# Kernel tuning notes

Hardware: AMD Instinct MI355X
Metric: run time of the kernel (lower is better)

Reference implementation:

```python
import jax, jax.numpy as jnp
import numpy as np

S, B, HQ, HK, D = 2048, 2, 32, 8, 128


def setup_inputs() -> dict:
    key = jax.random.key(0)
    kq, kk, kv = jax.random.split(key, 3)
    return {
        "query": jax.random.normal(kq, (S, B, HQ, D), dtype=jnp.float32),
        "key": jax.random.normal(kk, (S, B, HK, D), dtype=jnp.float32),
        "value": jax.random.normal(kv, (S, B, HK, D), dtype=jnp.float32),
    }


def reference(query, key, value):
    # s b h d -> b s h d (module's rearrange)
    q = jnp.transpose(query, (1, 0, 2, 3))  # [B,S,HQ,D]
    k = jnp.transpose(key, (1, 0, 2, 3))    # [B,S,HK,D]
    v = jnp.transpose(value, (1, 0, 2, 3))
    n_rep = q.shape[2] // k.shape[2]
    # repeat_kv: GQA expand along head dim (repeat_interleave semantics)
    k = jnp.repeat(k, n_rep, axis=2)  # [B,S,HQ,D]
    v = jnp.repeat(v, n_rep, axis=2)
    scale = q.shape[-1] ** -0.5
    # [B,H,Sq,Sk] scores; causal mask
    scores = jnp.einsum("bqhd,bkhd->bhqk", q, k) * scale
    s = scores.shape[-1]
    causal = jnp.tril(jnp.ones((s, s), dtype=bool))
    scores = jnp.where(causal[None, None], scores, jnp.finfo(scores.dtype).min)
    probs = jax.nn.softmax(scores, axis=-1)
    out = jnp.einsum("bhqk,bkhd->bqhd", probs, v)  # [B,S,H,D]
    # back to Megatron output layout [s, b, h*d]
    out = jnp.transpose(out, (1, 0, 2, 3))
    return out.reshape(out.shape[0], out.shape[1], -1)
```

## Files before the change

kernel.cpp:

```cpp
#include <hip/hip_runtime.h>

#define SLEN 2048
#define NB 2
#define NHQ 32
#define NHK 8
#define DH 128
#define QBLK 128
#define KVBLK 64
#define NT (SLEN / KVBLK)
#define NQT (SLEN / QBLK)
#define TILE_B (KVBLK * DH * 2)

typedef float  f32x4  __attribute__((ext_vector_type(4)));
typedef short  bf16x8 __attribute__((ext_vector_type(8)));

__device__ __forceinline__ unsigned short f2bf(float f) {
  union { float f; unsigned int u; } v; v.f = f;
  return (unsigned short)((v.u + 0x7fffu + ((v.u >> 16) & 1u)) >> 16);
}

__device__ __forceinline__ unsigned int cvtpk(float a, float b) {
  unsigned int r;
  asm("v_cvt_pk_bf16_f32 %0, %1, %2" : "=v"(r) : "v"(a), "v"(b));
  return r;
}

#define GLOAD16(g, l)                                                                   \
  __builtin_amdgcn_global_load_lds(                                                    \
      (const __attribute__((address_space(1))) unsigned int*)(g),                      \
      (__attribute__((address_space(3))) unsigned int*)(l), 16, 0, 0)

__global__ __launch_bounds__(256)
void prep_kv(const float* __restrict__ K, const float* __restrict__ V,
             unsigned short* __restrict__ W) {
  const int tile = blockIdx.x;
  const int bh   = blockIdx.y;
  const int tid  = threadIdx.x;
  const size_t krs = (size_t)NB * NHK * DH;
  const float* kb = K + (size_t)bh * DH + (size_t)tile * KVBLK * krs;
  const float* vb = V + (size_t)bh * DH + (size_t)tile * KVBLK * krs;
  unsigned short* kd = W + ((size_t)bh * NT + tile) * (KVBLK * DH);
  unsigned short* vd = W + (size_t)NB * NHK * NT * (KVBLK * DH)
                         + ((size_t)bh * NT + tile) * (KVBLK * DH);
#pragma unroll
  for (int i = 0; i < 4; ++i) {
    const int cid  = tid + 256 * i;
    const int row  = cid >> 4;
    const int cpos = (cid & 15) << 4;
    const int cb   = cpos ^ ((row & 7) << 4);
    const float* s = kb + (size_t)row * krs + (cb >> 1);
    float4 f0 = *(const float4*)s;
    float4 f1 = *(const float4*)(s + 4);
    bf16x8 a;
    a[0]=(short)f2bf(f0.x); a[1]=(short)f2bf(f0.y); a[2]=(short)f2bf(f0.z); a[3]=(short)f2bf(f0.w);
    a[4]=(short)f2bf(f1.x); a[5]=(short)f2bf(f1.y); a[6]=(short)f2bf(f1.z); a[7]=(short)f2bf(f1.w);
    *(bf16x8*)((char*)kd + row * 256 + cpos) = a;
  }
#pragma unroll
  for (int i = 0; i < 4; ++i) {
    const int cid  = tid + 256 * i;
    const int d    = cid >> 3;
    const int cpos = (cid & 7) << 4;
    const int kb2  = cpos ^ ((d & 7) << 4);
    const int p0   = kb2 >> 1;
    bf16x8 a;
#pragma unroll
    for (int j = 0; j < 8; ++j) {
      const int p  = p0 + j;
      const int kv = (p & 32) | ((p & 4) << 2) | ((p & 24) >> 1) | (p & 3);
      a[j] = (short)f2bf(vb[(size_t)kv * krs + d]);
    }
    *(bf16x8*)((char*)vd + d * 128 + cpos) = a;
  }
}

__global__ __launch_bounds__(256, 3)
void fattn_fwd(const float* __restrict__ Q, const unsigned short* __restrict__ KW,
               const unsigned short* __restrict__ VW, float* __restrict__ O) {
  const int tid  = threadIdx.x;
  const int w    = tid >> 6;
  const int lane = tid & 63;
  const int l15  = lane & 15;
  const int g    = lane >> 4;

  const int wg  = (int)blockIdx.x;
  const int xcd = wg & 7;
  const int c0  = wg >> 3;
  const int bh  = 8 * xcd + (c0 & 7);
  const int qt  = (NQT - 1) - (c0 >> 3);
  const int b   = bh >> 5;
  const int h   = bh & (NHQ - 1);
  const int kh  = h >> 2;

  __shared__ alignas(16) unsigned short Kbuf[2][KVBLK * DH];
  __shared__ alignas(16) unsigned short Vbuf[DH * KVBLK];

  const char* kws = (const char*)(KW + ((size_t)(b * NHK + kh) * NT) * (KVBLK * DH));
  const char* vws = (const char*)(VW + ((size_t)(b * NHK + kh) * NT) * (KVBLK * DH));

  const float sc = 0.08838834764831845f * 1.4426950408889634f;

  const int qs0 = qt * QBLK + 32 * w;
  const int nt  = 2 * qt + 2;

  bf16x8 qa[2][4];
#pragma unroll
  for (int u = 0; u < 2; ++u) {
    const float* qp = Q + ((size_t)((qs0 + 16 * u + l15) * NB + b) * NHQ + h) * DH;
#pragma unroll
    for (int s = 0; s < 4; ++s) {
      const float* p = qp + 32 * s + 8 * g;
      float4 f0 = *(const float4*)(p);
      float4 f1 = *(const float4*)(p + 4);
      bf16x8 a;
      a[0]=(short)f2bf(f0.x*sc); a[1]=(short)f2bf(f0.y*sc);
      a[2]=(short)f2bf(f0.z*sc); a[3]=(short)f2bf(f0.w*sc);
      a[4]=(short)f2bf(f1.x*sc); a[5]=(short)f2bf(f1.y*sc);
      a[6]=(short)f2bf(f1.z*sc); a[7]=(short)f2bf(f1.w*sc);
      qa[u][s] = a;
    }
  }

  bf16x8 ones;
#pragma unroll
  for (int i = 0; i < 8; ++i) ones[i] = (short)0x3F80;

  f32x4 o[2][8];
#pragma unroll
  for (int u = 0; u < 2; ++u)
#pragma unroll
    for (int dt = 0; dt < 8; ++dt) o[u][dt] = (f32x4){0.f, 0.f, 0.f, 0.f};
  f32x4 lacc[2] = {(f32x4){0.f,0.f,0.f,0.f}, (f32x4){0.f,0.f,0.f,0.f}};

#pragma unroll
  for (int i = 0; i < 4; ++i) {
    const int off = i * 4096 + w * 1024;
    GLOAD16(kws + off + (lane << 4), (char*)Kbuf[0] + off);
  }

  int cur = 0;
  for (int it = 0; it < nt; ++it) {
    {
      const char* vs = vws + (size_t)it * TILE_B;
#pragma unroll
      for (int i = 0; i < 4; ++i) {
        const int off = i * 4096 + w * 1024;
        GLOAD16(vs + off + (lane << 4), (char*)Vbuf + off);
      }
    }
    if (it + 1 < nt) {
      const char* ks = kws + (size_t)(it + 1) * TILE_B;
#pragma unroll
      for (int i = 0; i < 4; ++i) {
        const int off = i * 4096 + w * 1024;
        GLOAD16(ks + off + (lane << 4), (char*)Kbuf[cur ^ 1] + off);
      }
      asm volatile("s_waitcnt vmcnt(8)" ::: "memory");
    } else {
      asm volatile("s_waitcnt vmcnt(4)" ::: "memory");
    }
    __builtin_amdgcn_s_barrier();
    asm volatile("" ::: "memory");

    const unsigned short* Kc = Kbuf[cur];
    const int kv0 = it * KVBLK;
    const bool live = (kv0 <= qs0 + 31);

    f32x4 acc[2][4];
    bf16x8 pav[2][2];
    if (live) {
#pragma unroll
      for (int u = 0; u < 2; ++u)
#pragma unroll
        for (int c = 0; c < 4; ++c) acc[u][c] = (f32x4){0.f, 0.f, 0.f, 0.f};
      __builtin_amdgcn_s_setprio(1);
#pragma unroll
      for (int s = 0; s < 4; ++s) {
        const int cb = 64 * s + 16 * g;
#pragma unroll
        for (int c = 0; c < 4; ++c) {
          const int row = 16 * c + l15;
          bf16x8 kfr = *(const bf16x8*)((const char*)Kc + row * 256 + (cb ^ ((row & 7) << 4)));
          acc[0][c] = __builtin_amdgcn_mfma_f32_16x16x32_bf16(kfr, qa[0][s], acc[0][c], 0, 0, 0);
          acc[1][c] = __builtin_amdgcn_mfma_f32_16x16x32_bf16(kfr, qa[1][s], acc[1][c], 0, 0, 0);
        }
      }
      __builtin_amdgcn_s_setprio(0);

#pragma unroll
      for (int u = 0; u < 2; ++u) {
        const int qs   = qs0 + 16 * u;
        const int qrow = qs + l15;
        const bool domask = (kv0 + KVBLK - 1 > qs);
        float p[4][4];
#pragma unroll
        for (int c = 0; c < 4; ++c)
#pragma unroll
          for (int r = 0; r < 4; ++r) {
            float v = acc[u][c][r];
            if (domask) {
              const int kv = kv0 + 16 * c + 4 * g + r;
              v = (kv > qrow) ? -1e30f : v;
            }
            p[c][r] = exp2f(v);
          }

#pragma unroll
        for (int ks = 0; ks < 2; ++ks) {
          union { unsigned int u32[4]; bf16x8 v; } pu;
          pu.u32[0] = cvtpk(p[2 * ks][0], p[2 * ks][1]);
          pu.u32[1] = cvtpk(p[2 * ks][2], p[2 * ks][3]);
          pu.u32[2] = cvtpk(p[2 * ks + 1][0], p[2 * ks + 1][1]);
          pu.u32[3] = cvtpk(p[2 * ks + 1][2], p[2 * ks + 1][3]);
          pav[u][ks] = pu.v;
        }
      }

      lacc[0] = __builtin_amdgcn_mfma_f32_16x16x32_bf16(ones, pav[0][0], lacc[0], 0, 0, 0);
      lacc[0] = __builtin_amdgcn_mfma_f32_16x16x32_bf16(ones, pav[0][1], lacc[0], 0, 0, 0);
      lacc[1] = __builtin_amdgcn_mfma_f32_16x16x32_bf16(ones, pav[1][0], lacc[1], 0, 0, 0);
      lacc[1] = __builtin_amdgcn_mfma_f32_16x16x32_bf16(ones, pav[1][1], lacc[1], 0, 0, 0);
    }

    if (it + 1 < nt) {
      asm volatile("s_waitcnt vmcnt(4)" ::: "memory");
    } else {
      asm volatile("s_waitcnt vmcnt(0)" ::: "memory");
    }
    __builtin_amdgcn_s_barrier();
    asm volatile("" ::: "memory");

    if (live) {
      __builtin_amdgcn_s_setprio(1);
#pragma unroll
      for (int ks = 0; ks < 2; ++ks) {
#pragma unroll
        for (int dt = 0; dt < 8; ++dt) {
          const int d = 16 * dt + l15;
          bf16x8 vfr = *(const bf16x8*)((const char*)Vbuf + d * 128 +
                                        ((64 * ks + 16 * g) ^ ((d & 7) << 4)));
          o[0][dt] = __builtin_amdgcn_mfma_f32_16x16x32_bf16(vfr, pav[0][ks], o[0][dt], 0, 0, 0);
          o[1][dt] = __builtin_amdgcn_mfma_f32_16x16x32_bf16(vfr, pav[1][ks], o[1][dt], 0, 0, 0);
        }
      }
      __builtin_amdgcn_s_setprio(0);
    }

    asm volatile("" ::: "memory");
    __builtin_amdgcn_s_barrier();
    cur ^= 1;
  }

#pragma unroll
  for (int u = 0; u < 2; ++u) {
    const float rl = 1.0f / lacc[u][0];
    const int qrow = qs0 + 16 * u + l15;
    float* ob = O + ((size_t)b * NHQ + h) * DH + (size_t)qrow * (NB * NHQ * DH);
#pragma unroll
    for (int dt = 0; dt < 8; ++dt) {
      float4 st;
      st.x = o[u][dt][0] * rl; st.y = o[u][dt][1] * rl;
      st.z = o[u][dt][2] * rl; st.w = o[u][dt][3] * rl;
      *(float4*)(ob + 16 * dt + 4 * g) = st;
    }
  }
}

extern "C" void kernel_launch(void* const* d_in, const int* in_sizes, int n_in,
                              void* d_out, int out_size, void* d_ws, size_t ws_size,
                              hipStream_t stream) {
  const float* Q = (const float*)d_in[0];
  const float* K = (const float*)d_in[1];
  const float* V = (const float*)d_in[2];
  float* Out = (float*)d_out;
  unsigned short* W = (unsigned short*)d_ws;

  dim3 pgrid(NT, NB * NHK);
  prep_kv<<<pgrid, 256, 0, stream>>>(K, V, W);

  const unsigned short* KW = W;
  const unsigned short* VW = W + (size_t)NB * NHK * NT * (KVBLK * DH);
  fattn_fwd<<<dim3(NQT * NB * NHQ), 256, 0, stream>>>(Q, KW, VW, Out);
}
```

Measured before the change: 120.4 us.

## Split V tile into LDS-staged half and register-loaded half, double-buffer V

```diff
diff --git a/kernel.cpp b/kernel.cpp
--- a/kernel.cpp
+++ b/kernel.cpp
@@ -9,7 +9,8 @@
 #define KVBLK 64
 #define NT (SLEN / KVBLK)
 #define NQT (SLEN / QBLK)
-#define TILE_B (KVBLK * DH * 2)
+#define KTILE_B (KVBLK * DH * 2)
+#define VTILE_B (KVBLK * DH)
 
 typedef float  f32x4  __attribute__((ext_vector_type(4)));
 typedef short  bf16x8 __attribute__((ext_vector_type(8)));
@@ -32,16 +33,17 @@
 
 __global__ __launch_bounds__(256)
 void prep_kv(const float* __restrict__ K, const float* __restrict__ V,
-             unsigned short* __restrict__ W) {
+             unsigned short* __restrict__ KW, unsigned short* __restrict__ V0W,
+             unsigned short* __restrict__ V1W) {
   const int tile = blockIdx.x;
   const int bh   = blockIdx.y;
   const int tid  = threadIdx.x;
   const size_t krs = (size_t)NB * NHK * DH;
   const float* kb = K + (size_t)bh * DH + (size_t)tile * KVBLK * krs;
   const float* vb = V + (size_t)bh * DH + (size_t)tile * KVBLK * krs;
-  unsigned short* kd = W + ((size_t)bh * NT + tile) * (KVBLK * DH);
-  unsigned short* vd = W + (size_t)NB * NHK * NT * (KVBLK * DH)
-                         + ((size_t)bh * NT + tile) * (KVBLK * DH);
+  unsigned short* kd  = KW  + ((size_t)bh * NT + tile) * (KVBLK * DH);
+  unsigned short* v0d = V0W + ((size_t)bh * NT + tile) * (KVBLK * DH / 2);
+  unsigned short* v1d = V1W + ((size_t)bh * NT + tile) * (KVBLK * DH / 2);
 #pragma unroll
   for (int i = 0; i < 4; ++i) {
     const int cid  = tid + 256 * i;
@@ -58,25 +60,35 @@
   }
 #pragma unroll
   for (int i = 0; i < 4; ++i) {
-    const int cid  = tid + 256 * i;
-    const int d    = cid >> 3;
-    const int cpos = (cid & 7) << 4;
-    const int kb2  = cpos ^ ((d & 7) << 4);
-    const int p0   = kb2 >> 1;
+    const int cid = tid + 256 * i;
+    const int d   = cid >> 3;
+    const int ch  = cid & 7;
     bf16x8 a;
-#pragma unroll
-    for (int j = 0; j < 8; ++j) {
-      const int p  = p0 + j;
-      const int kv = (p & 32) | ((p & 4) << 2) | ((p & 24) >> 1) | (p & 3);
-      a[j] = (short)f2bf(vb[(size_t)kv * krs + d]);
-    }
-    *(bf16x8*)((char*)vd + d * 128 + cpos) = a;
+    if (ch < 4) {
+#pragma unroll
+      for (int jj = 0; jj < 8; ++jj) {
+        const int s2 = 8 * ch + jj;
+        const int kv = ((s2 & 4) << 2) | ((s2 & 24) >> 1) | (s2 & 3);
+        a[jj] = (short)f2bf(vb[(size_t)kv * krs + d]);
+      }
+      *(bf16x8*)((char*)v0d + d * 64 + ((ch ^ (d & 3)) << 4)) = a;
+    } else {
+      const int j = ch - 4;
+#pragma unroll
+      for (int jj = 0; jj < 8; ++jj) {
+        const int s2 = 8 * j + jj;
+        const int kv = 32 | (((s2 & 4) << 2) | ((s2 & 24) >> 1) | (s2 & 3));
+        a[jj] = (short)f2bf(vb[(size_t)kv * krs + d]);
+      }
+      *(bf16x8*)((char*)v1d + d * 64 + (j << 4)) = a;
+    }
   }
 }
 
 __global__ __launch_bounds__(256, 3)
 void fattn_fwd(const float* __restrict__ Q, const unsigned short* __restrict__ KW,
-               const unsigned short* __restrict__ VW, float* __restrict__ O) {
+               const unsigned short* __restrict__ V0W, const unsigned short* __restrict__ V1W,
+               float* __restrict__ O) {
   const int tid  = threadIdx.x;
   const int w    = tid >> 6;
   const int lane = tid & 63;
@@ -93,10 +105,11 @@
   const int kh  = h >> 2;
 
   __shared__ alignas(16) unsigned short Kbuf[2][KVBLK * DH];
-  __shared__ alignas(16) unsigned short Vbuf[DH * KVBLK];
-
-  const char* kws = (const char*)(KW + ((size_t)(b * NHK + kh) * NT) * (KVBLK * DH));
-  const char* vws = (const char*)(VW + ((size_t)(b * NHK + kh) * NT) * (KVBLK * DH));
+  __shared__ alignas(16) unsigned short V0buf[2][DH * (KVBLK / 2)];
+
+  const char* kws  = (const char*)(KW  + ((size_t)(b * NHK + kh) * NT) * (KVBLK * DH));
+  const char* v0ws = (const char*)(V0W + ((size_t)(b * NHK + kh) * NT) * (KVBLK * DH / 2));
+  const char* v1ws = (const char*)(V1W + ((size_t)(b * NHK + kh) * NT) * (KVBLK * DH / 2));
 
   const float sc = 0.08838834764831845f * 1.4426950408889634f;
 
@@ -137,28 +150,35 @@
     const int off = i * 4096 + w * 1024;
     GLOAD16(kws + off + (lane << 4), (char*)Kbuf[0] + off);
   }
+#pragma unroll
+  for (int i = 0; i < 2; ++i) {
+    const int off = i * 4096 + w * 1024;
+    GLOAD16(v0ws + off + (lane << 4), (char*)V0buf[0] + off);
+  }
 
   int cur = 0;
   for (int it = 0; it < nt; ++it) {
+    const char* yb = v1ws + (size_t)it * VTILE_B + (l15 * 64 + 16 * g);
+    bf16x8 Y[8];
+#pragma unroll
+    for (int dt = 0; dt < 8; ++dt) Y[dt] = *(const bf16x8*)(yb + 1024 * dt);
+
+    const int pf = (it + 1 < nt) ? it + 1 : it;
     {
-      const char* vs = vws + (size_t)it * TILE_B;
-#pragma unroll
-      for (int i = 0; i < 4; ++i) {
-        const int off = i * 4096 + w * 1024;
-        GLOAD16(vs + off + (lane << 4), (char*)Vbuf + off);
-      }
-    }
-    if (it + 1 < nt) {
-      const char* ks = kws + (size_t)(it + 1) * TILE_B;
+      const char* ks = kws + (size_t)pf * KTILE_B;
+      const char* vs = v0ws + (size_t)pf * VTILE_B;
 #pragma unroll
       for (int i = 0; i < 4; ++i) {
         const int off = i * 4096 + w * 1024;
         GLOAD16(ks + off + (lane << 4), (char*)Kbuf[cur ^ 1] + off);
       }
-      asm volatile("s_waitcnt vmcnt(8)" ::: "memory");
-    } else {
-      asm volatile("s_waitcnt vmcnt(4)" ::: "memory");
-    }
+#pragma unroll
+      for (int i = 0; i < 2; ++i) {
+        const int off = i * 4096 + w * 1024;
+        GLOAD16(vs + off + (lane << 4), (char*)V0buf[cur ^ 1] + off);
+      }
+    }
+    asm volatile("s_waitcnt vmcnt(14)" ::: "memory");
     __builtin_amdgcn_s_barrier();
     asm volatile("" ::: "memory");
 
@@ -166,9 +186,9 @@
     const int kv0 = it * KVBLK;
     const bool live = (kv0 <= qs0 + 31);
 
-    f32x4 acc[2][4];
     bf16x8 pav[2][2];
     if (live) {
+      f32x4 acc[2][4];
 #pragma unroll
       for (int u = 0; u < 2; ++u)
 #pragma unroll
@@ -204,7 +224,6 @@
             }
             p[c][r] = exp2f(v);
           }
-
 #pragma unroll
         for (int ks = 0; ks < 2; ++ks) {
           union { unsigned int u32[4]; bf16x8 v; } pu;
@@ -220,28 +239,26 @@
       lacc[0] = __builtin_amdgcn_mfma_f32_16x16x32_bf16(ones, pav[0][1], lacc[0], 0, 0, 0);
       lacc[1] = __builtin_amdgcn_mfma_f32_16x16x32_bf16(ones, pav[1][0], lacc[1], 0, 0, 0);
       lacc[1] = __builtin_amdgcn_mfma_f32_16x16x32_bf16(ones, pav[1][1], lacc[1], 0, 0, 0);
-    }
-
-    if (it + 1 < nt) {
-      asm volatile("s_waitcnt vmcnt(4)" ::: "memory");
-    } else {
-      asm volatile("s_waitcnt vmcnt(0)" ::: "memory");
-    }
-    __builtin_amdgcn_s_barrier();
-    asm volatile("" ::: "memory");
-
+
+      __builtin_amdgcn_s_setprio(1);
+#pragma unroll
+      for (int dt = 0; dt < 8; ++dt) {
+        const int d = 16 * dt + l15;
+        bf16x8 vfr = *(const bf16x8*)((const char*)V0buf[cur] + d * 64 +
+                                      ((g ^ (d & 3)) << 4));
+        o[0][dt] = __builtin_amdgcn_mfma_f32_16x16x32_bf16(vfr, pav[0][0], o[0][dt], 0, 0, 0);
+        o[1][dt] = __builtin_amdgcn_mfma_f32_16x16x32_bf16(vfr, pav[1][0], o[1][dt], 0, 0, 0);
+      }
+      __builtin_amdgcn_s_setprio(0);
+    }
+
+    asm volatile("s_waitcnt vmcnt(6)" ::: "memory");
     if (live) {
       __builtin_amdgcn_s_setprio(1);
 #pragma unroll
-      for (int ks = 0; ks < 2; ++ks) {
-#pragma unroll
-        for (int dt = 0; dt < 8; ++dt) {
-          const int d = 16 * dt + l15;
-          bf16x8 vfr = *(const bf16x8*)((const char*)Vbuf + d * 128 +
-                                        ((64 * ks + 16 * g) ^ ((d & 7) << 4)));
-          o[0][dt] = __builtin_amdgcn_mfma_f32_16x16x32_bf16(vfr, pav[0][ks], o[0][dt], 0, 0, 0);
-          o[1][dt] = __builtin_amdgcn_mfma_f32_16x16x32_bf16(vfr, pav[1][ks], o[1][dt], 0, 0, 0);
-        }
+      for (int dt = 0; dt < 8; ++dt) {
+        o[0][dt] = __builtin_amdgcn_mfma_f32_16x16x32_bf16(Y[dt], pav[0][1], o[0][dt], 0, 0, 0);
+        o[1][dt] = __builtin_amdgcn_mfma_f32_16x16x32_bf16(Y[dt], pav[1][1], o[1][dt], 0, 0, 0);
       }
       __builtin_amdgcn_s_setprio(0);
     }
@@ -250,6 +267,8 @@
     __builtin_amdgcn_s_barrier();
     cur ^= 1;
   }
+
+  asm volatile("s_waitcnt vmcnt(0)" ::: "memory");
 
 #pragma unroll
   for (int u = 0; u < 2; ++u) {
@@ -275,10 +294,12 @@
   float* Out = (float*)d_out;
   unsigned short* W = (unsigned short*)d_ws;
 
+  unsigned short* KW  = W;
+  unsigned short* V0W = KW + (size_t)NB * NHK * NT * (KVBLK * DH);
+  unsigned short* V1W = V0W + (size_t)NB * NHK * NT * (KVBLK * DH / 2);
+
   dim3 pgrid(NT, NB * NHK);
-  prep_kv<<<pgrid, 256, 0, stream>>>(K, V, W);
-
-  const unsigned short* KW = W;
-  const unsigned short* VW = W + (size_t)NB * NHK * NT * (KVBLK * DH);
-  fattn_fwd<<<dim3(NQT * NB * NHQ), 256, 0, stream>>>(Q, KW, VW, Out);
-}
+  prep_kv<<<pgrid, 256, 0, stream>>>(K, V, KW, V0W, V1W);
+
+  fattn_fwd<<<dim3(NQT * NB * NHQ), 256, 0, stream>>>(Q, KW, V0W, V1W, Out);
+}
```

New measurement: 278.8 us. +131.6%, slower.

## Triple-buffer K/V tiles in LDS and prefetch next V during PV

Applied to the files above, without the earlier changes.

```diff
diff --git a/kernel.cpp b/kernel.cpp
--- a/kernel.cpp
+++ b/kernel.cpp
@@ -92,8 +92,7 @@
   const int h   = bh & (NHQ - 1);
   const int kh  = h >> 2;
 
-  __shared__ alignas(16) unsigned short Kbuf[2][KVBLK * DH];
-  __shared__ alignas(16) unsigned short Vbuf[DH * KVBLK];
+  __shared__ alignas(16) unsigned short Buf[3][KVBLK * DH];
 
   const char* kws = (const char*)(KW + ((size_t)(b * NHK + kh) * NT) * (KVBLK * DH));
   const char* vws = (const char*)(VW + ((size_t)(b * NHK + kh) * NT) * (KVBLK * DH));
@@ -102,6 +101,12 @@
 
   const int qs0 = qt * QBLK + 32 * w;
   const int nt  = 2 * qt + 2;
+
+  const int xm   = (l15 & 7) << 4;
+  const char* kb0 = (const char*)Buf[0] + l15 * 256 + ((16 * g) ^ xm);
+  const char* kb1 = kb0 + (64 - ((l15 & 4) << 5));
+  const char* vb0 = (const char*)Buf[0] + l15 * 128 + ((16 * g) ^ xm);
+  const char* vb1 = vb0 + (64 - ((l15 & 4) << 5));
 
   bf16x8 qa[2][4];
 #pragma unroll
@@ -135,121 +140,126 @@
 #pragma unroll
   for (int i = 0; i < 4; ++i) {
     const int off = i * 4096 + w * 1024;
-    GLOAD16(kws + off + (lane << 4), (char*)Kbuf[0] + off);
-  }
-
-  int cur = 0;
-  for (int it = 0; it < nt; ++it) {
-    {
-      const char* vs = vws + (size_t)it * TILE_B;
-#pragma unroll
-      for (int i = 0; i < 4; ++i) {
-        const int off = i * 4096 + w * 1024;
-        GLOAD16(vs + off + (lane << 4), (char*)Vbuf + off);
-      }
-    }
-    if (it + 1 < nt) {
-      const char* ks = kws + (size_t)(it + 1) * TILE_B;
-#pragma unroll
-      for (int i = 0; i < 4; ++i) {
-        const int off = i * 4096 + w * 1024;
-        GLOAD16(ks + off + (lane << 4), (char*)Kbuf[cur ^ 1] + off);
-      }
-      asm volatile("s_waitcnt vmcnt(8)" ::: "memory");
-    } else {
-      asm volatile("s_waitcnt vmcnt(4)" ::: "memory");
-    }
-    __builtin_amdgcn_s_barrier();
-    asm volatile("" ::: "memory");
-
-    const unsigned short* Kc = Kbuf[cur];
-    const int kv0 = it * KVBLK;
-    const bool live = (kv0 <= qs0 + 31);
-
-    f32x4 acc[2][4];
-    bf16x8 pav[2][2];
-    if (live) {
-#pragma unroll
-      for (int u = 0; u < 2; ++u)
-#pragma unroll
-        for (int c = 0; c < 4; ++c) acc[u][c] = (f32x4){0.f, 0.f, 0.f, 0.f};
-      __builtin_amdgcn_s_setprio(1);
-#pragma unroll
-      for (int s = 0; s < 4; ++s) {
-        const int cb = 64 * s + 16 * g;
-#pragma unroll
-        for (int c = 0; c < 4; ++c) {
-          const int row = 16 * c + l15;
-          bf16x8 kfr = *(const bf16x8*)((const char*)Kc + row * 256 + (cb ^ ((row & 7) << 4)));
-          acc[0][c] = __builtin_amdgcn_mfma_f32_16x16x32_bf16(kfr, qa[0][s], acc[0][c], 0, 0, 0);
-          acc[1][c] = __builtin_amdgcn_mfma_f32_16x16x32_bf16(kfr, qa[1][s], acc[1][c], 0, 0, 0);
-        }
-      }
-      __builtin_amdgcn_s_setprio(0);
-
-#pragma unroll
-      for (int u = 0; u < 2; ++u) {
-        const int qs   = qs0 + 16 * u;
-        const int qrow = qs + l15;
-        const bool domask = (kv0 + KVBLK - 1 > qs);
-        float p[4][4];
-#pragma unroll
-        for (int c = 0; c < 4; ++c)
-#pragma unroll
-          for (int r = 0; r < 4; ++r) {
-            float v = acc[u][c][r];
-            if (domask) {
-              const int kv = kv0 + 16 * c + 4 * g + r;
-              v = (kv > qrow) ? -1e30f : v;
-            }
-            p[c][r] = exp2f(v);
-          }
-
-#pragma unroll
-        for (int ks = 0; ks < 2; ++ks) {
-          union { unsigned int u32[4]; bf16x8 v; } pu;
-          pu.u32[0] = cvtpk(p[2 * ks][0], p[2 * ks][1]);
-          pu.u32[1] = cvtpk(p[2 * ks][2], p[2 * ks][3]);
-          pu.u32[2] = cvtpk(p[2 * ks + 1][0], p[2 * ks + 1][1]);
-          pu.u32[3] = cvtpk(p[2 * ks + 1][2], p[2 * ks + 1][3]);
-          pav[u][ks] = pu.v;
-        }
-      }
-
-      lacc[0] = __builtin_amdgcn_mfma_f32_16x16x32_bf16(ones, pav[0][0], lacc[0], 0, 0, 0);
-      lacc[0] = __builtin_amdgcn_mfma_f32_16x16x32_bf16(ones, pav[0][1], lacc[0], 0, 0, 0);
-      lacc[1] = __builtin_amdgcn_mfma_f32_16x16x32_bf16(ones, pav[1][0], lacc[1], 0, 0, 0);
-      lacc[1] = __builtin_amdgcn_mfma_f32_16x16x32_bf16(ones, pav[1][1], lacc[1], 0, 0, 0);
-    }
-
-    if (it + 1 < nt) {
-      asm volatile("s_waitcnt vmcnt(4)" ::: "memory");
-    } else {
-      asm volatile("s_waitcnt vmcnt(0)" ::: "memory");
-    }
-    __builtin_amdgcn_s_barrier();
-    asm volatile("" ::: "memory");
-
-    if (live) {
-      __builtin_amdgcn_s_setprio(1);
-#pragma unroll
-      for (int ks = 0; ks < 2; ++ks) {
-#pragma unroll
-        for (int dt = 0; dt < 8; ++dt) {
-          const int d = 16 * dt + l15;
-          bf16x8 vfr = *(const bf16x8*)((const char*)Vbuf + d * 128 +
-                                        ((64 * ks + 16 * g) ^ ((d & 7) << 4)));
-          o[0][dt] = __builtin_amdgcn_mfma_f32_16x16x32_bf16(vfr, pav[0][ks], o[0][dt], 0, 0, 0);
-          o[1][dt] = __builtin_amdgcn_mfma_f32_16x16x32_bf16(vfr, pav[1][ks], o[1][dt], 0, 0, 0);
-        }
-      }
-      __builtin_amdgcn_s_setprio(0);
-    }
-
-    asm volatile("" ::: "memory");
-    __builtin_amdgcn_s_barrier();
-    cur ^= 1;
-  }
+    GLOAD16(kws + off + (lane << 4), (char*)Buf[0] + off);
+  }
+#pragma unroll
+  for (int i = 0; i < 4; ++i) {
+    const int off = i * 4096 + w * 1024;
+    GLOAD16(vws + off + (lane << 4), (char*)Buf[2] + off);
+  }
+
+  int it = 0;
+
+#define ITER(KB, VB)                                                                    \
+  {                                                                                     \
+                                                    \
+    if (it + 1 < nt) {                                                                  \
+      const char* ks_ = kws + (size_t)(it + 1) * TILE_B;                                \
+      _Pragma("unroll")                                                                 \
+      for (int i = 0; i < 4; ++i) {                                                     \
+        const int off = i * 4096 + w * 1024;                                            \
+        GLOAD16(ks_ + off + (lane << 4), (char*)Buf[(KB + 1) % 3] + off);               \
+      }                                                                                 \
+      asm volatile("s_waitcnt vmcnt(8)" ::: "memory");                 \
+    } else {                                                                            \
+      asm volatile("s_waitcnt vmcnt(4)" ::: "memory");          \
+    }                                                                                   \
+    __builtin_amdgcn_s_barrier();                          \
+    asm volatile("" ::: "memory");                                                      \
+    const int kv0 = it * KVBLK;                                                         \
+    const bool live = (kv0 <= qs0 + 31);                                                \
+    bf16x8 pav[2][2];                                                                   \
+    if (live) {                                                                         \
+      f32x4 acc[2][4];                                                                  \
+      _Pragma("unroll")                                                                 \
+      for (int u = 0; u < 2; ++u)                                                       \
+        _Pragma("unroll")                                                               \
+        for (int c = 0; c < 4; ++c) acc[u][c] = (f32x4){0.f, 0.f, 0.f, 0.f};            \
+      __builtin_amdgcn_s_setprio(1);                                                    \
+      _Pragma("unroll")                                                                 \
+      for (int s = 0; s < 4; ++s) {                                                     \
+        const char* kp = (s & 1) ? kb1 : kb0;                                           \
+        _Pragma("unroll")                                                               \
+        for (int c = 0; c < 4; ++c) {                                                   \
+          bf16x8 kfr = *(const bf16x8*)(kp + (KB) * 16384 + (s >> 1) * 128 + c * 4096); \
+          acc[0][c] = __builtin_amdgcn_mfma_f32_16x16x32_bf16(kfr, qa[0][s], acc[0][c], 0, 0, 0); \
+          acc[1][c] = __builtin_amdgcn_mfma_f32_16x16x32_bf16(kfr, qa[1][s], acc[1][c], 0, 0, 0); \
+        }                                                                               \
+      }                                                                                 \
+      __builtin_amdgcn_s_setprio(0);                                                    \
+      _Pragma("unroll")                                                                 \
+      for (int u = 0; u < 2; ++u) {                                                     \
+        const int qs   = qs0 + 16 * u;                                                  \
+        const int qrow = qs + l15;                                                      \
+        const bool domask = (kv0 + KVBLK - 1 > qs);                                     \
+        float p[4][4];                                                                  \
+        _Pragma("unroll")                                                               \
+        for (int c = 0; c < 4; ++c)                                                     \
+          _Pragma("unroll")                                                             \
+          for (int r = 0; r < 4; ++r) {                                                 \
+            float v = acc[u][c][r];                                                     \
+            if (domask) {                                                               \
+              const int kv = kv0 + 16 * c + 4 * g + r;                                  \
+              v = (kv > qrow) ? -1e30f : v;                                             \
+            }                                                                           \
+            p[c][r] = exp2f(v);                                                         \
+          }                                                                             \
+        _Pragma("unroll")                                                               \
+        for (int ks2 = 0; ks2 < 2; ++ks2) {                                             \
+          union { unsigned int u32[4]; bf16x8 v; } pu;                                  \
+          pu.u32[0] = cvtpk(p[2 * ks2][0], p[2 * ks2][1]);                              \
+          pu.u32[1] = cvtpk(p[2 * ks2][2], p[2 * ks2][3]);                              \
+          pu.u32[2] = cvtpk(p[2 * ks2 + 1][0], p[2 * ks2 + 1][1]);                      \
+          pu.u32[3] = cvtpk(p[2 * ks2 + 1][2], p[2 * ks2 + 1][3]);                      \
+          pav[u][ks2] = pu.v;                                                           \
+        }                                                                               \
+      }                                                                                 \
+      lacc[0] = __builtin_amdgcn_mfma_f32_16x16x32_bf16(ones, pav[0][0], lacc[0], 0, 0, 0); \
+      lacc[0] = __builtin_amdgcn_mfma_f32_16x16x32_bf16(ones, pav[0][1], lacc[0], 0, 0, 0); \
+      lacc[1] = __builtin_amdgcn_mfma_f32_16x16x32_bf16(ones, pav[1][0], lacc[1], 0, 0, 0); \
+      lacc[1] = __builtin_amdgcn_mfma_f32_16x16x32_bf16(ones, pav[1][1], lacc[1], 0, 0, 0); \
+    }                                                                                   \
+                  \
+    if (it + 1 < nt) {                                                                  \
+      asm volatile("s_waitcnt vmcnt(4)" ::: "memory");                                  \
+    } else {                                                                            \
+      asm volatile("s_waitcnt vmcnt(0)" ::: "memory");                                  \
+    }                                                                                   \
+    __builtin_amdgcn_s_barrier();       \
+    asm volatile("" ::: "memory");                                                      \
+            \
+    if (it + 1 < nt) {                                                                  \
+      const char* vs_ = vws + (size_t)(it + 1) * TILE_B;                                \
+      _Pragma("unroll")                                                                 \
+      for (int i = 0; i < 4; ++i) {                                                     \
+        const int off = i * 4096 + w * 1024;                                            \
+        GLOAD16(vs_ + off + (lane << 4), (char*)Buf[KB] + off);                         \
+      }                                                                                 \
+    }                                                                                   \
+    if (live) {                                                                         \
+      __builtin_amdgcn_s_setprio(1);                                                    \
+      _Pragma("unroll")                                                                 \
+      for (int ks2 = 0; ks2 < 2; ++ks2) {                                               \
+        const char* vp = ks2 ? vb1 : vb0;                                               \
+        _Pragma("unroll")                                                               \
+        for (int dt = 0; dt < 8; ++dt) {                                                \
+          bf16x8 vfr = *(const bf16x8*)(vp + (VB) * 16384 + dt * 2048);                 \
+          o[0][dt] = __builtin_amdgcn_mfma_f32_16x16x32_bf16(vfr, pav[0][ks2], o[0][dt], 0, 0, 0); \
+          o[1][dt] = __builtin_amdgcn_mfma_f32_16x16x32_bf16(vfr, pav[1][ks2], o[1][dt], 0, 0, 0); \
+        }                                                                               \
+      }                                                                                 \
+      __builtin_amdgcn_s_setprio(0);                                                    \
+    }                                                                                   \
+    asm volatile("" ::: "memory");                                                      \
+    __builtin_amdgcn_s_barrier();       \
+  }
+
+  while (true) {
+    ITER(0, 2); if (++it == nt) break;
+    ITER(1, 0); if (++it == nt) break;
+    ITER(2, 1); if (++it == nt) break;
+  }
+#undef ITER
 
 #pragma unroll
   for (int u = 0; u < 2; ++u) {
```

New measurement: 282.5 us. 2.35x slower.
